# Kernel optimization log

Hardware: AMD Instinct MI355X
Metric: run time of the kernel (lower is better)

## Reference

```python
import jax, jax.numpy as jnp
import numpy as np

K, R, D = 200000, 64, 1024
N_IDS = 16384
BITS = 4
GROUP = 32


def group_quantize(w, bits, group_size):
    """Group-wise symmetric fake-quant along the last dim (STE in bwd)."""
    last = w.shape[-1]
    g = min(group_size, last)
    n_groups = last // g
    wg = w.reshape(w.shape[:-1] + (n_groups, g))
    amax = jnp.clip(jnp.max(jnp.abs(wg), axis=-1, keepdims=True), 1e-8, None)
    q_max = (1 << (bits - 1)) - 1  # matches torch `1 << bits - 1` precedence
    scale = amax / q_max
    q = jnp.clip(jnp.round(wg / scale), -q_max, q_max) * scale
    # straight-through estimator: forward = q, backward = identity w.r.t. wg
    wq = wg + jax.lax.stop_gradient(q - wg)
    return wq.reshape(w.shape)


def setup_inputs() -> dict:
    key = jax.random.key(0)
    k1, k2, k3 = jax.random.split(key, 3)
    U = jax.random.normal(k1, (K, R), dtype=jnp.float32)
    B = jax.random.normal(k2, (R, D), dtype=jnp.float32)
    local_ids = jax.random.randint(k3, (N_IDS,), 0, K, dtype=jnp.int64 if jax.config.read('jax_enable_x64') else jnp.int32)
    return {"U": U, "B": B, "local_ids": local_ids}


def reference(U, B, local_ids):
    # row(): quantize ALL of U, gather selected rows, matmul with quantized B
    Uq = group_quantize(U, BITS, min(GROUP, R))   # [K, r]
    Bq = group_quantize(B, BITS, min(GROUP, D))   # [r, d]
    return Uq[local_ids] @ Bq                      # [N, d]
```

## Files before the change

kernel.cpp:

```cpp
#include <hip/hip_runtime.h>


#define R_DIM 64
#define D_DIM 1024
#define N_IDS 16384

#define BM 128
#define BN 128
#define LDS_STRIDE 72
#define OT_STRIDE 132

typedef __attribute__((ext_vector_type(8))) __bf16 bf16x8;
typedef __attribute__((ext_vector_type(4))) float f32x4;

__device__ inline unsigned short f32_to_bf16_rne(float f) {
  union { float f; unsigned int u; } c; c.f = f;
  unsigned int u = c.u;
  u += 0x7fffu + ((u >> 16) & 1u);
  return (unsigned short)(u >> 16);
}

__device__ inline float bf16_bits_to_f32(unsigned short h) {
  union { unsigned int u; float f; } c; c.u = ((unsigned int)h) << 16;
  return c.f;
}

__device__ inline void quant_elem(float w, double scale,
                                  unsigned short* hi, unsigned short* lo) {
  double t = (double)w / scale;
  double q = fmin(fmax(rint(t), -7.0), 7.0) * scale;
  float qf = (float)q;
  unsigned short h = f32_to_bf16_rne(qf);
  *hi = h;
  *lo = f32_to_bf16_rne(qf - bf16_bits_to_f32(h));
}

__global__ __launch_bounds__(256) void quantB_kernel(
    const float* __restrict__ B,
    unsigned short* __restrict__ BqT_hi, unsigned short* __restrict__ BqT_lo) {
  int e4 = blockIdx.x * 256 + threadIdx.x;
  int e  = e4 * 4;
  int r  = e >> 10;
  int c  = e & 1023;
  float4 w = *(const float4*)(B + e);
  float a = fmaxf(fmaxf(fabsf(w.x), fabsf(w.y)), fmaxf(fabsf(w.z), fabsf(w.w)));
  a = fmaxf(a, __shfl_xor(a, 1));
  a = fmaxf(a, __shfl_xor(a, 2));
  a = fmaxf(a, __shfl_xor(a, 4));
  double sc = fmax((double)a, 1e-8) / 7.0;
  float wv[4] = {w.x, w.y, w.z, w.w};
  #pragma unroll
  for (int j = 0; j < 4; ++j) {
    unsigned short hi, lo;
    quant_elem(wv[j], sc, &hi, &lo);
    BqT_hi[(c + j) * R_DIM + r] = hi;
    BqT_lo[(c + j) * R_DIM + r] = lo;
  }
}

__global__ __launch_bounds__(256, 4) void gemm_kernel(
    const float* __restrict__ U, const int* __restrict__ ids,
    const unsigned short* __restrict__ BqT_hi, const unsigned short* __restrict__ BqT_lo,
    float* __restrict__ out) {
  __shared__ char smem[2 * BN * LDS_STRIDE * 2];
  unsigned short* bt_hi = (unsigned short*)smem;
  unsigned short* bt_lo = bt_hi + BN * LDS_STRIDE;
  float* ot = (float*)smem;

  const int tid  = threadIdx.x;
  const int lane = tid & 63;
  const int wave = tid >> 6;
  const int bx   = blockIdx.x;
  const int nb   = bx & 7;
  const int mb   = bx >> 3;
  const int n0   = nb * BN;
  const int m0b  = mb * BM;
  const int koff  = (lane >> 4) * 8;
  const int nlane = lane & 15;

  const float* urow0 = U + (size_t)ids[m0b + wave * 16 + nlane] * R_DIM;
  const float* urow1 = U + (size_t)ids[m0b + 64 + wave * 16 + nlane] * R_DIM;
  float4 wr[2][2][2];
  #pragma unroll
  for (int s = 0; s < 2; ++s) {
    wr[0][s][0] = *(const float4*)(urow0 + s * 32 + koff);
    wr[0][s][1] = *(const float4*)(urow0 + s * 32 + koff + 4);
    wr[1][s][0] = *(const float4*)(urow1 + s * 32 + koff);
    wr[1][s][1] = *(const float4*)(urow1 + s * 32 + koff + 4);
  }

  {
    const uint4* src_hi = (const uint4*)(BqT_hi + (size_t)n0 * R_DIM);
    const uint4* src_lo = (const uint4*)(BqT_lo + (size_t)n0 * R_DIM);
    #pragma unroll
    for (int it = 0; it < 4; ++it) {
      int c = tid + it * 256;
      int row = c >> 3, off = c & 7;
      *(uint4*)&bt_hi[row * LDS_STRIDE + off * 8] = src_hi[c];
      *(uint4*)&bt_lo[row * LDS_STRIDE + off * 8] = src_lo[c];
    }
  }

  bf16x8 ah[2][2], al[2][2];
  #pragma unroll
  for (int mf = 0; mf < 2; ++mf) {
    #pragma unroll
    for (int s = 0; s < 2; ++s) {
      float4 w0 = wr[mf][s][0], w1 = wr[mf][s][1];
      float wv[8] = {w0.x, w0.y, w0.z, w0.w, w1.x, w1.y, w1.z, w1.w};
      float a = 0.0f;
      #pragma unroll
      for (int j = 0; j < 8; ++j) a = fmaxf(a, fabsf(wv[j]));
      a = fmaxf(a, __shfl_xor(a, 16));
      a = fmaxf(a, __shfl_xor(a, 32));
      double sc = fmax((double)a, 1e-8) / 7.0;
      union { unsigned short s8[8]; bf16x8 b; } uh, ul;
      #pragma unroll
      for (int j = 0; j < 8; ++j) {
        unsigned short hi, lo;
        quant_elem(wv[j], sc, &hi, &lo);
        uh.s8[j] = hi;
        ul.s8[j] = lo;
      }
      ah[mf][s] = uh.b;
      al[mf][s] = ul.b;
    }
  }

  __syncthreads();

  f32x4 acc[2][8];
  #pragma unroll
  for (int mf = 0; mf < 2; ++mf)
    #pragma unroll
    for (int nf = 0; nf < 8; ++nf) acc[mf][nf] = (f32x4){0.f, 0.f, 0.f, 0.f};

  #pragma unroll
  for (int nf = 0; nf < 8; ++nf) {
    #pragma unroll
    for (int s = 0; s < 2; ++s) {
      const int boff = (nf * 16 + nlane) * LDS_STRIDE + s * 32 + koff;
      union { uint4 u; bf16x8 b; } bh, bl;
      bh.u = *(const uint4*)&bt_hi[boff];
      bl.u = *(const uint4*)&bt_lo[boff];
      #pragma unroll
      for (int mf = 0; mf < 2; ++mf) {
        acc[mf][nf] = __builtin_amdgcn_mfma_f32_16x16x32_bf16(ah[mf][s], bh.b, acc[mf][nf], 0, 0, 0);
        acc[mf][nf] = __builtin_amdgcn_mfma_f32_16x16x32_bf16(ah[mf][s], bl.b, acc[mf][nf], 0, 0, 0);
        acc[mf][nf] = __builtin_amdgcn_mfma_f32_16x16x32_bf16(al[mf][s], bh.b, acc[mf][nf], 0, 0, 0);
      }
    }
  }

  __syncthreads();

  float* wp = ot + wave * 16 * OT_STRIDE;
  #pragma unroll
  for (int mf = 0; mf < 2; ++mf) {
    const int r0 = (lane >> 4) << 2;
    #pragma unroll
    for (int nf = 0; nf < 8; ++nf) {
      #pragma unroll
      for (int i = 0; i < 4; ++i) {
        wp[(r0 + i) * OT_STRIDE + nlane + nf * 16] = acc[mf][nf][i];
      }
    }
    const int orow0 = m0b + mf * 64 + wave * 16;
    #pragma unroll
    for (int j = 0; j < 8; ++j) {
      const int row = j * 2 + (lane >> 5);
      f32x4 v = *(const f32x4*)&wp[row * OT_STRIDE + (lane & 31) * 4];
      __builtin_nontemporal_store(v,
          (f32x4*)&out[(size_t)(orow0 + row) * D_DIM + n0 + (lane & 31) * 4]);
    }
  }
}

extern "C" void kernel_launch(void* const* d_in, const int* in_sizes, int n_in,
                              void* d_out, int out_size, void* d_ws, size_t ws_size,
                              hipStream_t stream) {
  const float* U   = (const float*)d_in[0];
  const float* B   = (const float*)d_in[1];
  const int*   ids = (const int*)d_in[2];
  float* out = (float*)d_out;

  unsigned short* BqT_hi = (unsigned short*)d_ws;
  unsigned short* BqT_lo = BqT_hi + R_DIM * D_DIM;

  quantB_kernel<<<(R_DIM * D_DIM) / (256 * 4), 256, 0, stream>>>(B, BqT_hi, BqT_lo);
  gemm_kernel<<<(N_IDS / BM) * (D_DIM / BN), 256, 0, stream>>>(U, ids, BqT_hi, BqT_lo, out);
}
```

Baseline: 27.47 us.

## Fuse B quantization into GEMM kernel and drop separate quant launch

Removes the standalone B-quantization kernel and workspace round trip. Each GEMM block now loads its 64x128 slice of B in fp32, computes the per-group scales, quantizes into hi/lo bf16 and writes the transposed result straight to LDS. Block index mapping is also swapped so consecutive blocks share the same N tile, which is meant to improve L2 reuse of B. This removes a kernel launch and its dependency, but every block now repeats the quantization with double-precision math and does scattered 2-byte LDS writes.

Result: slower. 29.02 us (+5.6%).

```diff
diff --git a/kernel.cpp b/kernel.cpp
--- a/kernel.cpp
+++ b/kernel.cpp
@@ -35,33 +35,9 @@
   *lo = f32_to_bf16_rne(qf - bf16_bits_to_f32(h));
 }
 
-__global__ __launch_bounds__(256) void quantB_kernel(
-    const float* __restrict__ B,
-    unsigned short* __restrict__ BqT_hi, unsigned short* __restrict__ BqT_lo) {
-  int e4 = blockIdx.x * 256 + threadIdx.x;
-  int e  = e4 * 4;
-  int r  = e >> 10;
-  int c  = e & 1023;
-  float4 w = *(const float4*)(B + e);
-  float a = fmaxf(fmaxf(fabsf(w.x), fabsf(w.y)), fmaxf(fabsf(w.z), fabsf(w.w)));
-  a = fmaxf(a, __shfl_xor(a, 1));
-  a = fmaxf(a, __shfl_xor(a, 2));
-  a = fmaxf(a, __shfl_xor(a, 4));
-  double sc = fmax((double)a, 1e-8) / 7.0;
-  float wv[4] = {w.x, w.y, w.z, w.w};
-  #pragma unroll
-  for (int j = 0; j < 4; ++j) {
-    unsigned short hi, lo;
-    quant_elem(wv[j], sc, &hi, &lo);
-    BqT_hi[(c + j) * R_DIM + r] = hi;
-    BqT_lo[(c + j) * R_DIM + r] = lo;
-  }
-}
-
 __global__ __launch_bounds__(256, 4) void gemm_kernel(
-    const float* __restrict__ U, const int* __restrict__ ids,
-    const unsigned short* __restrict__ BqT_hi, const unsigned short* __restrict__ BqT_lo,
-    float* __restrict__ out) {
+    const float* __restrict__ U, const float* __restrict__ B,
+    const int* __restrict__ ids, float* __restrict__ out) {
   __shared__ char smem[2 * BN * LDS_STRIDE * 2];
   unsigned short* bt_hi = (unsigned short*)smem;
   unsigned short* bt_lo = bt_hi + BN * LDS_STRIDE;
@@ -71,8 +47,8 @@
   const int lane = tid & 63;
   const int wave = tid >> 6;
   const int bx   = blockIdx.x;
-  const int nb   = bx & 7;
-  const int mb   = bx >> 3;
+  const int mb   = bx & 127;
+  const int nb   = bx >> 7;
   const int n0   = nb * BN;
   const int m0b  = mb * BM;
   const int koff  = (lane >> 4) * 8;
@@ -90,14 +66,28 @@
   }
 
   {
-    const uint4* src_hi = (const uint4*)(BqT_hi + (size_t)n0 * R_DIM);
-    const uint4* src_lo = (const uint4*)(BqT_lo + (size_t)n0 * R_DIM);
+    const int r = tid >> 2, g = tid & 3;
+    const float* bp = B + (size_t)r * D_DIM + n0 + g * 32;
+    float4 bv[8];
     #pragma unroll
-    for (int it = 0; it < 4; ++it) {
-      int c = tid + it * 256;
-      int row = c >> 3, off = c & 7;
-      *(uint4*)&bt_hi[row * LDS_STRIDE + off * 8] = src_hi[c];
-      *(uint4*)&bt_lo[row * LDS_STRIDE + off * 8] = src_lo[c];
+    for (int q = 0; q < 8; ++q) bv[q] = *(const float4*)(bp + q * 4);
+    float a = 0.0f;
+    #pragma unroll
+    for (int q = 0; q < 8; ++q)
+      a = fmaxf(a, fmaxf(fmaxf(fabsf(bv[q].x), fabsf(bv[q].y)),
+                         fmaxf(fabsf(bv[q].z), fabsf(bv[q].w))));
+    double sc = fmax((double)a, 1e-8) / 7.0;
+    #pragma unroll
+    for (int q = 0; q < 8; ++q) {
+      float wv[4] = {bv[q].x, bv[q].y, bv[q].z, bv[q].w};
+      #pragma unroll
+      for (int j = 0; j < 4; ++j) {
+        unsigned short hi, lo;
+        quant_elem(wv[j], sc, &hi, &lo);
+        const int c = g * 32 + q * 4 + j;
+        bt_hi[c * LDS_STRIDE + r] = hi;
+        bt_lo[c * LDS_STRIDE + r] = lo;
+      }
     }
   }
 
@@ -184,9 +174,5 @@
   const int*   ids = (const int*)d_in[2];
   float* out = (float*)d_out;
 
-  unsigned short* BqT_hi = (unsigned short*)d_ws;
-  unsigned short* BqT_lo = BqT_hi + R_DIM * D_DIM;
-
-  quantB_kernel<<<(R_DIM * D_DIM) / (256 * 4), 256, 0, stream>>>(B, BqT_hi, BqT_lo);
-  gemm_kernel<<<(N_IDS / BM) * (D_DIM / BN), 256, 0, stream>>>(U, ids, BqT_hi, BqT_lo, out);
+  gemm_kernel<<<(N_IDS / BM) * (D_DIM / BN), 256, 0, stream>>>(U, B, ids, out);
 }
```

## Shrink GEMM tiles to 64x64, read B fragments directly from global, drop LDS

Applied to the files above, without the earlier changes.

Reduces the block tile from 128x128 to 64x64 and raises the occupancy hint. The LDS staging of the quantized B tile and the LDS transpose of the output are removed. Each wave now loads its B fragments straight from global memory, which should hit L2 since BqT is only 256 KB. Outputs are written as scalar nontemporal stores instead of float4 stores. This removes both barriers and the LDS traffic but quadruples the block count, re-quantizes more U rows per output, and makes the output stores narrower and less coalesced, so write efficiency may drop on a store-bound kernel.

Result: slower. 52.03 us (+89.4%).

```diff
diff --git a/kernel.cpp b/kernel.cpp
--- a/kernel.cpp
+++ b/kernel.cpp
@@ -5,10 +5,8 @@
 #define D_DIM 1024
 #define N_IDS 16384
 
-#define BM 128
-#define BN 128
-#define LDS_STRIDE 72
-#define OT_STRIDE 132
+#define BM 64
+#define BN 64
 
 typedef __attribute__((ext_vector_type(8))) __bf16 bf16x8;
 typedef __attribute__((ext_vector_type(4))) float f32x4;
@@ -58,120 +56,77 @@
   }
 }
 
-__global__ __launch_bounds__(256, 4) void gemm_kernel(
+__global__ __launch_bounds__(256, 8) void gemm_kernel(
     const float* __restrict__ U, const int* __restrict__ ids,
     const unsigned short* __restrict__ BqT_hi, const unsigned short* __restrict__ BqT_lo,
     float* __restrict__ out) {
-  __shared__ char smem[2 * BN * LDS_STRIDE * 2];
-  unsigned short* bt_hi = (unsigned short*)smem;
-  unsigned short* bt_lo = bt_hi + BN * LDS_STRIDE;
-  float* ot = (float*)smem;
-
   const int tid  = threadIdx.x;
   const int lane = tid & 63;
   const int wave = tid >> 6;
   const int bx   = blockIdx.x;
-  const int nb   = bx & 7;
-  const int mb   = bx >> 3;
+  const int nb   = bx & 15;
+  const int mb   = bx >> 4;
   const int n0   = nb * BN;
-  const int m0b  = mb * BM;
+  const int m0   = mb * BM + wave * 16;
   const int koff  = (lane >> 4) * 8;
   const int nlane = lane & 15;
 
-  const float* urow0 = U + (size_t)ids[m0b + wave * 16 + nlane] * R_DIM;
-  const float* urow1 = U + (size_t)ids[m0b + 64 + wave * 16 + nlane] * R_DIM;
-  float4 wr[2][2][2];
+  const float* urow = U + (size_t)ids[m0 + nlane] * R_DIM;
+  float4 wr[2][2];
   #pragma unroll
   for (int s = 0; s < 2; ++s) {
-    wr[0][s][0] = *(const float4*)(urow0 + s * 32 + koff);
-    wr[0][s][1] = *(const float4*)(urow0 + s * 32 + koff + 4);
-    wr[1][s][0] = *(const float4*)(urow1 + s * 32 + koff);
-    wr[1][s][1] = *(const float4*)(urow1 + s * 32 + koff + 4);
+    wr[s][0] = *(const float4*)(urow + s * 32 + koff);
+    wr[s][1] = *(const float4*)(urow + s * 32 + koff + 4);
   }
 
-  {
-    const uint4* src_hi = (const uint4*)(BqT_hi + (size_t)n0 * R_DIM);
-    const uint4* src_lo = (const uint4*)(BqT_lo + (size_t)n0 * R_DIM);
+  bf16x8 ah[2], al[2];
+  #pragma unroll
+  for (int s = 0; s < 2; ++s) {
+    float4 w0 = wr[s][0], w1 = wr[s][1];
+    float wv[8] = {w0.x, w0.y, w0.z, w0.w, w1.x, w1.y, w1.z, w1.w};
+    float a = 0.0f;
     #pragma unroll
-    for (int it = 0; it < 4; ++it) {
-      int c = tid + it * 256;
-      int row = c >> 3, off = c & 7;
-      *(uint4*)&bt_hi[row * LDS_STRIDE + off * 8] = src_hi[c];
-      *(uint4*)&bt_lo[row * LDS_STRIDE + off * 8] = src_lo[c];
+    for (int j = 0; j < 8; ++j) a = fmaxf(a, fabsf(wv[j]));
+    a = fmaxf(a, __shfl_xor(a, 16));
+    a = fmaxf(a, __shfl_xor(a, 32));
+    double sc = fmax((double)a, 1e-8) / 7.0;
+    union { unsigned short s8[8]; bf16x8 b; } uh, ul;
+    #pragma unroll
+    for (int j = 0; j < 8; ++j) {
+      unsigned short hi, lo;
+      quant_elem(wv[j], sc, &hi, &lo);
+      uh.s8[j] = hi;
+      ul.s8[j] = lo;
+    }
+    ah[s] = uh.b;
+    al[s] = ul.b;
+  }
+
+  f32x4 acc[4];
+  #pragma unroll
+  for (int nf = 0; nf < 4; ++nf) acc[nf] = (f32x4){0.f, 0.f, 0.f, 0.f};
+
+  #pragma unroll
+  for (int nf = 0; nf < 4; ++nf) {
+    const size_t brow = (size_t)(n0 + nf * 16 + nlane) * R_DIM;
+    #pragma unroll
+    for (int s = 0; s < 2; ++s) {
+      bf16x8 bh = *(const bf16x8*)&BqT_hi[brow + s * 32 + koff];
+      bf16x8 bl = *(const bf16x8*)&BqT_lo[brow + s * 32 + koff];
+      acc[nf] = __builtin_amdgcn_mfma_f32_16x16x32_bf16(ah[s], bh, acc[nf], 0, 0, 0);
+      acc[nf] = __builtin_amdgcn_mfma_f32_16x16x32_bf16(ah[s], bl, acc[nf], 0, 0, 0);
+      acc[nf] = __builtin_amdgcn_mfma_f32_16x16x32_bf16(al[s], bh, acc[nf], 0, 0, 0);
     }
   }
 
-  bf16x8 ah[2][2], al[2][2];
+  const int orow0 = m0 + ((lane >> 4) << 2);
   #pragma unroll
-  for (int mf = 0; mf < 2; ++mf) {
+  for (int nf = 0; nf < 4; ++nf) {
+    const int ocol = n0 + nf * 16 + nlane;
     #pragma unroll
-    for (int s = 0; s < 2; ++s) {
-      float4 w0 = wr[mf][s][0], w1 = wr[mf][s][1];
-      float wv[8] = {w0.x, w0.y, w0.z, w0.w, w1.x, w1.y, w1.z, w1.w};
-      float a = 0.0f;
-      #pragma unroll
-      for (int j = 0; j < 8; ++j) a = fmaxf(a, fabsf(wv[j]));
-      a = fmaxf(a, __shfl_xor(a, 16));
-      a = fmaxf(a, __shfl_xor(a, 32));
-      double sc = fmax((double)a, 1e-8) / 7.0;
-      union { unsigned short s8[8]; bf16x8 b; } uh, ul;
-      #pragma unroll
-      for (int j = 0; j < 8; ++j) {
-        unsigned short hi, lo;
-        quant_elem(wv[j], sc, &hi, &lo);
-        uh.s8[j] = hi;
-        ul.s8[j] = lo;
-      }
-      ah[mf][s] = uh.b;
-      al[mf][s] = ul.b;
-    }
-  }
-
-  __syncthreads();
-
-  f32x4 acc[2][8];
-  #pragma unroll
-  for (int mf = 0; mf < 2; ++mf)
-    #pragma unroll
-    for (int nf = 0; nf < 8; ++nf) acc[mf][nf] = (f32x4){0.f, 0.f, 0.f, 0.f};
-
-  #pragma unroll
-  for (int nf = 0; nf < 8; ++nf) {
-    #pragma unroll
-    for (int s = 0; s < 2; ++s) {
-      const int boff = (nf * 16 + nlane) * LDS_STRIDE + s * 32 + koff;
-      union { uint4 u; bf16x8 b; } bh, bl;
-      bh.u = *(const uint4*)&bt_hi[boff];
-      bl.u = *(const uint4*)&bt_lo[boff];
-      #pragma unroll
-      for (int mf = 0; mf < 2; ++mf) {
-        acc[mf][nf] = __builtin_amdgcn_mfma_f32_16x16x32_bf16(ah[mf][s], bh.b, acc[mf][nf], 0, 0, 0);
-        acc[mf][nf] = __builtin_amdgcn_mfma_f32_16x16x32_bf16(ah[mf][s], bl.b, acc[mf][nf], 0, 0, 0);
-        acc[mf][nf] = __builtin_amdgcn_mfma_f32_16x16x32_bf16(al[mf][s], bh.b, acc[mf][nf], 0, 0, 0);
-      }
-    }
-  }
-
-  __syncthreads();
-
-  float* wp = ot + wave * 16 * OT_STRIDE;
-  #pragma unroll
-  for (int mf = 0; mf < 2; ++mf) {
-    const int r0 = (lane >> 4) << 2;
-    #pragma unroll
-    for (int nf = 0; nf < 8; ++nf) {
-      #pragma unroll
-      for (int i = 0; i < 4; ++i) {
-        wp[(r0 + i) * OT_STRIDE + nlane + nf * 16] = acc[mf][nf][i];
-      }
-    }
-    const int orow0 = m0b + mf * 64 + wave * 16;
-    #pragma unroll
-    for (int j = 0; j < 8; ++j) {
-      const int row = j * 2 + (lane >> 5);
-      f32x4 v = *(const f32x4*)&wp[row * OT_STRIDE + (lane & 31) * 4];
-      __builtin_nontemporal_store(v,
-          (f32x4*)&out[(size_t)(orow0 + row) * D_DIM + n0 + (lane & 31) * 4]);
+    for (int i = 0; i < 4; ++i) {
+      __builtin_nontemporal_store(acc[nf][i],
+          &out[(size_t)(orow0 + i) * D_DIM + ocol]);
     }
   }
 }
```
